# Kernel optimization log

Hardware: AMD Instinct MI355X
Metric: run time of the kernel (lower is better)

## Reference

```python
import jax, jax.numpy as jnp
import numpy as np

E = 1024  # embed_dim
H = 16    # heads
D = E // H            # head_dim = 64
M = 4 * D             # nb_features = 256
B, N = 4, 4096
KERNEL_EPS = 1e-4


def setup_inputs() -> dict:
    key = jax.random.key(0)
    ks = jax.random.split(key, 7)
    s = E ** -0.5
    return {
        "x": jax.random.normal(ks[0], (B, N, E), jnp.float32),
        "Wq": jax.random.normal(ks[1], (E, E), jnp.float32) * s,
        "bq": jnp.zeros((E,), jnp.float32),
        "Wk": jax.random.normal(ks[2], (E, E), jnp.float32) * s,
        "bk": jnp.zeros((E,), jnp.float32),
        "Wv": jax.random.normal(ks[3], (E, E), jnp.float32) * s,
        "bv": jnp.zeros((E,), jnp.float32),
        "Wo": jax.random.normal(ks[4], (E, E), jnp.float32) * s,
        "bo": jnp.zeros((E,), jnp.float32),
        "proj": jax.random.normal(ks[5], (M, D), jnp.float32),  # FAVOR+ random features
    }


def softmax_kernel(data, proj, is_query):
    # data: [B,H,N,D], proj: [M,D] -> features [B,H,N,M]
    d = data.shape[-1]
    data_n = data * (d ** -0.25)
    ratio = proj.shape[0] ** -0.5
    dd = jnp.einsum('bhnd,md->bhnm', data_n, proj)
    diag = 0.5 * jnp.sum(data_n * data_n, axis=-1, keepdims=True)
    if is_query:
        stab = jnp.max(dd, axis=-1, keepdims=True)
    else:
        stab = jnp.max(dd)
    return ratio * (jnp.exp(dd - diag - stab) + KERNEL_EPS)


def reference(x, Wq, bq, Wk, bk, Wv, bv, Wo, bo, proj):
    b, n, e = x.shape
    def split_heads(t):
        return t.reshape(b, n, H, D).transpose(0, 2, 1, 3)  # [B,H,N,D]
    q = split_heads(x @ Wq.T + bq)
    k = split_heads(x @ Wk.T + bk)
    v = split_heads(x @ Wv.T + bv)

    qf = softmax_kernel(q, proj, is_query=True)   # [B,H,N,M]
    kf = softmax_kernel(k, proj, is_query=False)  # [B,H,N,M]

    # non-causal linear attention: O(N*M*D)
    k_sum = jnp.sum(kf, axis=-2)                          # [B,H,M]
    d_inv = 1.0 / jnp.einsum('bhnm,bhm->bhn', qf, k_sum)  # [B,H,N]
    context = jnp.einsum('bhnm,bhnd->bhmd', kf, v)        # [B,H,M,D]
    out = jnp.einsum('bhnm,bhmd,bhn->bhnd', qf, context, d_inv)

    out = out.transpose(0, 2, 1, 3).reshape(b, n, e)
    return out @ Wo.T + bo
```

## Files before the change

kernel.cpp:

```cpp
#include <hip/hip_runtime.h>
#include <hip/hip_bf16.h>
#include <stdint.h>


#define TOKN  16384
#define SEQ   4096
#define EMB   1024
#define LDQ   3072
#define NHEAD 16
#define HD    64
#define NF    256
#define BHN   64

static __device__ __forceinline__ constexpr float c1f()  { return 0.35355339059327379f; }
static __device__ __forceinline__ constexpr float ratf() { return 0.0625f; }
static __device__ __forceinline__ constexpr float kepsf(){ return 1e-4f; }

typedef unsigned short u16;
typedef unsigned int   u32;
typedef __attribute__((ext_vector_type(8))) short bf16x8;
typedef __attribute__((ext_vector_type(4))) float f32x4;
typedef __attribute__((ext_vector_type(4))) u16   u16x4;

union U8 { bf16x8 v8; u16x4 q[2]; };

__device__ __forceinline__ float bf2f(u16 u) { return __uint_as_float(((u32)u) << 16); }
__device__ __forceinline__ u16 f2bf(float f) {
  u32 u = __float_as_uint(f);
  u += 0x7fffu + ((u >> 16) & 1u);
  return (u16)(u >> 16);
}
__device__ __forceinline__ u32 encf(float f) {
  u32 u = __float_as_uint(f);
  return (u & 0x80000000u) ? ~u : (u | 0x80000000u);
}
__device__ __forceinline__ float decf(u32 e) {
  u32 u = (e & 0x80000000u) ? (e & 0x7fffffffu) : ~e;
  return __uint_as_float(u);
}

__device__ __forceinline__ void gl2lds16(const u16* g, void* l) {
  __builtin_amdgcn_global_load_lds(
      (const __attribute__((address_space(1))) u32*)g,
      (__attribute__((address_space(3))) u32*)l, 16, 0, 0);
}

#define ZERO_ACC(acc)                         \
  _Pragma("unroll") for (int _i = 0; _i < 4; _i++) \
  _Pragma("unroll") for (int _j = 0; _j < 4; _j++) acc[_i][_j] = (f32x4)0.0f;

template <int BM, int BN>
__device__ __forceinline__ void gemm_core(const u16* __restrict__ Ag, long lda,
                                          const u16* __restrict__ Bg, long ldb,
                                          int K, u16* sA, u16* sB,
                                          f32x4 (&acc)[4][4]) {
  const int tid = threadIdx.x;
  const int w = tid >> 6, l = tid & 63;
  constexpr int WM = BM / 64;
  const int wm = w % WM, wn = w / WM;
  const int lrow = l & 15, g4 = l >> 4;
  constexpr int AI = (BM * 8) / 256;
  constexpr int BI = (BN * 8) / 256;
  static_assert(AI + BI == 8, "vmcnt(8) literal assumes 8 loads/thread/tile");
  constexpr int ABUF = BM * 64;
  constexpr int BBUF = BN * 64;

  auto stage = [&](int k0, int sel) {
#pragma unroll
    for (int i = 0; i < AI; i++) {
      int q = i * 256 + tid;
      int row = q >> 3, part = (q & 7) ^ (row & 7);
      gl2lds16(Ag + (long)row * lda + k0 + part * 8,
               (char*)(sA + sel * ABUF) + i * 4096 + w * 1024);
    }
#pragma unroll
    for (int i = 0; i < BI; i++) {
      int q = i * 256 + tid;
      int row = q >> 3, part = (q & 7) ^ (row & 7);
      gl2lds16(Bg + (long)row * ldb + k0 + part * 8,
               (char*)(sB + sel * BBUF) + i * 4096 + w * 1024);
    }
  };

  stage(0, 0);
  const int NT = K >> 6;
  for (int t = 0; t < NT; ++t) {
    const int sel = t & 1;
    if (t + 1 < NT) {
      stage((t + 1) * 64, sel ^ 1);
      asm volatile("s_waitcnt vmcnt(8)" ::: "memory");
    } else {
      asm volatile("s_waitcnt vmcnt(0)" ::: "memory");
    }
    __builtin_amdgcn_s_barrier();
    __builtin_amdgcn_sched_barrier(0);
    const u16* pA = sA + sel * ABUF;
    const u16* pB = sB + sel * BBUF;
#pragma unroll
    for (int kk = 0; kk < 2; kk++) {
      bf16x8 af[4], bfr[4];
#pragma unroll
      for (int mt = 0; mt < 4; mt++) {
        int row = wm * 64 + mt * 16 + lrow;
        af[mt] = *(const bf16x8*)(pA + row * 64 + (((kk * 4 + g4) ^ (row & 7)) * 8));
      }
#pragma unroll
      for (int nt = 0; nt < 4; nt++) {
        int row = wn * 64 + nt * 16 + lrow;
        bfr[nt] = *(const bf16x8*)(pB + row * 64 + (((kk * 4 + g4) ^ (row & 7)) * 8));
      }
#pragma unroll
      for (int mt = 0; mt < 4; mt++)
#pragma unroll
        for (int nt = 0; nt < 4; nt++)
          acc[mt][nt] = __builtin_amdgcn_mfma_f32_16x16x32_bf16(af[mt], bfr[nt], acc[mt][nt], 0, 0, 0);
    }
    __builtin_amdgcn_s_barrier();
  }
}

template <bool BF16OUT>
__global__ __launch_bounds__(256) void k_gemm(const u16* __restrict__ A, const u16* __restrict__ Bw,
                                              void* __restrict__ Cout, const float* __restrict__ bias,
                                              int K, int lda, int ldb, int ldc) {
  __shared__ __align__(16) u16 sA[2 * 128 * 64];
  __shared__ __align__(16) u16 sB[2 * 128 * 64];
  const int nbx = gridDim.x;
  const int nwg = nbx * gridDim.y;
  int lin = blockIdx.y * nbx + blockIdx.x;
  if ((nwg & 7) == 0) {
    int per = nwg >> 3;
    lin = (lin & 7) * per + (lin >> 3);
  }
  const int m0 = (lin / nbx) * 128, n0 = (lin % nbx) * 128;
  f32x4 acc[4][4]; ZERO_ACC(acc);
  gemm_core<128, 128>(A + (long)m0 * lda, lda, Bw + (long)n0 * ldb, ldb, K, sA, sB, acc);
  const int l = threadIdx.x & 63, w = threadIdx.x >> 6;
  const int wm = w & 1, wn = w >> 1, lr4 = (l >> 4) * 4, lc = l & 15;
#pragma unroll
  for (int nt = 0; nt < 4; nt++) {
    int gcol = n0 + wn * 64 + nt * 16 + lc;
    float bia = bias[gcol];
#pragma unroll
    for (int mt = 0; mt < 4; mt++)
#pragma unroll
      for (int r = 0; r < 4; r++) {
        int grow = m0 + wm * 64 + mt * 16 + lr4 + r;
        float v = acc[mt][nt][r] + bia;
        if (BF16OUT) ((u16*)Cout)[(long)grow * ldc + gcol] = f2bf(v);
        else         ((float*)Cout)[(long)grow * ldc + gcol] = v;
      }
  }
}

__global__ __launch_bounds__(256) void k_gemm3(const u16* __restrict__ A, const u16* __restrict__ Bw,
                                               u16* __restrict__ Cout,
                                               const float* __restrict__ b0, const float* __restrict__ b1,
                                               const float* __restrict__ b2,
                                               int K, int lda, int ldb, int ldc) {
  __shared__ __align__(16) u16 sA[2 * 128 * 64];
  __shared__ __align__(16) u16 sB[2 * 128 * 64];
  const int nbx = gridDim.x;
  const int nwg = nbx * gridDim.y;
  int lin = blockIdx.y * nbx + blockIdx.x;
  if ((nwg & 7) == 0) {
    int per = nwg >> 3;
    lin = (lin & 7) * per + (lin >> 3);
  }
  const int m0 = (lin / nbx) * 128, n0 = (lin % nbx) * 128;
  f32x4 acc[4][4]; ZERO_ACC(acc);
  gemm_core<128, 128>(A + (long)m0 * lda, lda, Bw + (long)n0 * ldb, ldb, K, sA, sB, acc);
  const int l = threadIdx.x & 63, w = threadIdx.x >> 6;
  const int wm = w & 1, wn = w >> 1, lr4 = (l >> 4) * 4, lc = l & 15;
  const int seg = n0 >> 10;
  const float* bias = seg == 0 ? b0 : (seg == 1 ? b1 : b2);
#pragma unroll
  for (int nt = 0; nt < 4; nt++) {
    int gcol = n0 + wn * 64 + nt * 16 + lc;
    float bia = bias[gcol & 1023];
#pragma unroll
    for (int mt = 0; mt < 4; mt++)
#pragma unroll
      for (int r = 0; r < 4; r++) {
        int grow = m0 + wm * 64 + mt * 16 + lr4 + r;
        Cout[(long)grow * ldc + gcol] = f2bf(acc[mt][nt][r] + bia);
      }
  }
}

__global__ __launch_bounds__(256) void k_vT(const u16* __restrict__ vb, u16* __restrict__ vT,
                                            float* __restrict__ vsum) {
  __shared__ u16 t[64][72];
  const int bh = blockIdx.y, n0 = blockIdx.x * 64, b = bh >> 4, h = bh & 15;
  const int tid = threadIdx.x;
#pragma unroll
  for (int i = 0; i < 2; i++) {
    int idx = i * 256 + tid, row = idx >> 3, c8 = idx & 7;
    U8 u;
    u.v8 = *(const bf16x8*)&vb[((long)(b * SEQ) + n0 + row) * LDQ + h * HD + c8 * 8];
    *(u16x4*)&t[row][c8 * 8]     = u.q[0];
    *(u16x4*)&t[row][c8 * 8 + 4] = u.q[1];
  }
  __syncthreads();
  const int nq = tid & 15, dh = tid >> 4;
#pragma unroll
  for (int i = 0; i < 4; i++) {
    int d = i * 16 + dh;
    u16x4 pk; float s = 0.f;
#pragma unroll
    for (int j = 0; j < 4; j++) { u16 v = t[nq * 4 + j][d]; pk[j] = v; s += bf2f(v); }
    *(u16x4*)&vT[((long)bh * HD + d) * SEQ + n0 + nq * 4] = pk;
    s += __shfl_xor(s, 1); s += __shfl_xor(s, 2);
    s += __shfl_xor(s, 4); s += __shfl_xor(s, 8);
    if (nq == 0) atomicAdd(&vsum[bh * HD + d], s);
  }
}

__global__ __launch_bounds__(256, 2) void k_fk_ctx(const u16* __restrict__ kb, const u16* __restrict__ vT,
                                                   const u16* __restrict__ projb, u16* __restrict__ part,
                                                   float* __restrict__ su, u32* __restrict__ stabEnc) {
  __shared__ __align__(16) u16 sU[4][64 * 64];
  const int ck = blockIdx.x, bh = blockIdx.y, b = bh >> 4, h = bh & 15;
  const int tid = threadIdx.x, w = tid >> 6, l = tid & 63;
  const int c = l & 15, g = l >> 4;
  u16* sUw = &sU[w][0];
  const int sw = c & 7;

  bf16x8 pf[4][2];
#pragma unroll
  for (int nt = 0; nt < 4; nt++)
#pragma unroll
    for (int k0 = 0; k0 < 2; k0++)
      pf[nt][k0] = *(const bf16x8*)&projb[(w * 64 + nt * 16 + c) * 64 + k0 * 32 + g * 8];

  f32x4 acc2[4][4]; ZERO_ACC(acc2);
  float suv[4] = {0.f, 0.f, 0.f, 0.f};
  float amax = -1e30f;
  const long tok0 = (long)b * SEQ + ck * 256;

  for (int s = 0; s < 4; s++) {
    const long t0 = tok0 + s * 64;
    bf16x8 af[4][2];
#pragma unroll
    for (int mt = 0; mt < 4; mt++)
#pragma unroll
      for (int k0 = 0; k0 < 2; k0++)
        af[mt][k0] = *(const bf16x8*)&kb[(t0 + mt * 16 + c) * LDQ + h * HD + k0 * 32 + g * 8];
    bf16x8 vf[2][4];
#pragma unroll
    for (int k0 = 0; k0 < 2; k0++)
#pragma unroll
      for (int nt = 0; nt < 4; nt++)
        vf[k0][nt] = *(const bf16x8*)&vT[((long)bh * HD + nt * 16 + c) * SEQ +
                                         ck * 256 + s * 64 + k0 * 32 + g * 8];

#pragma unroll
    for (int mt = 0; mt < 4; mt++) {
      float ss = 0.f;
#pragma unroll
      for (int k0 = 0; k0 < 2; k0++)
#pragma unroll
        for (int j = 0; j < 8; j++) {
          float v = bf2f((u16)af[mt][k0][j]);
          ss += v * v;
        }
      ss += __shfl_xor(ss, 16);
      ss += __shfl_xor(ss, 32);
      const float dgrow = ss * 0.0625f;
      f32x4 accR[4];
#pragma unroll
      for (int nt = 0; nt < 4; nt++) accR[nt] = (f32x4)0.0f;
#pragma unroll
      for (int k0 = 0; k0 < 2; k0++)
#pragma unroll
        for (int nt = 0; nt < 4; nt++)
          accR[nt] = __builtin_amdgcn_mfma_f32_16x16x32_bf16(af[mt][k0], pf[nt][k0], accR[nt], 0, 0, 0);
      float dg[4];
#pragma unroll
      for (int r = 0; r < 4; r++) dg[r] = __shfl(dgrow, g * 4 + r);
#pragma unroll
      for (int nt = 0; nt < 4; nt++) {
        u16x4 pk;
#pragma unroll
        for (int r = 0; r < 4; r++) {
          float a = accR[nt][r];
          amax = fmaxf(amax, a);
          float U = __expf(fmaf(a, c1f(), -dg[r]));
          pk[r] = f2bf(U);
          suv[nt] += U;
        }
        *(u16x4*)&sUw[(nt * 16 + c) * 64 + (((mt * 2 + (g >> 1)) ^ sw) * 2 + (g & 1)) * 4] = pk;
      }
    }
#pragma unroll
    for (int k0 = 0; k0 < 2; k0++) {
      bf16x8 uf[4];
#pragma unroll
      for (int mt = 0; mt < 4; mt++)
        uf[mt] = *(const bf16x8*)&sUw[(mt * 16 + c) * 64 + ((k0 * 4 + g) ^ sw) * 8];
#pragma unroll
      for (int mt = 0; mt < 4; mt++)
#pragma unroll
        for (int nt = 0; nt < 4; nt++)
          acc2[mt][nt] = __builtin_amdgcn_mfma_f32_16x16x32_bf16(uf[mt], vf[k0][nt], acc2[mt][nt], 0, 0, 0);
    }
  }
  const long zp = (long)(bh * 16 + ck);
#pragma unroll
  for (int mt = 0; mt < 4; mt++)
#pragma unroll
    for (int nt = 0; nt < 4; nt++)
#pragma unroll
      for (int r = 0; r < 4; r++) {
        int m = w * 64 + mt * 16 + g * 4 + r;
        int d = nt * 16 + c;
        part[(zp * NF + m) * HD + d] = f2bf(acc2[mt][nt][r]);
      }
#pragma unroll
  for (int nt = 0; nt < 4; nt++) {
    float v = suv[nt];
    v += __shfl_xor(v, 16);
    v += __shfl_xor(v, 32);
    if (l < 16) atomicAdd(&su[bh * NF + w * 64 + nt * 16 + l], v);
  }
  for (int o = 32; o; o >>= 1) amax = fmaxf(amax, __shfl_xor(amax, o));
  if (l == 0) atomicMax(stabEnc, encf(c1f() * amax));
}

__global__ __launch_bounds__(256, 4) void k_fq_attn(const u16* __restrict__ qb, const u16* __restrict__ projb,
                                                    const float* __restrict__ k_sum, const float* __restrict__ ksum_tot,
                                                    const u16* __restrict__ ct_bf, const float* __restrict__ ctsum,
                                                    u16* __restrict__ attn_bf) {
  __shared__ __align__(16) u16 sUq[64 * 256];
  __shared__ float redmax[4][64];
  __shared__ float redsum[4][64];
  const int bh = blockIdx.y, b = bh >> 4, h = bh & 15;
  const long t0 = (long)b * SEQ + blockIdx.x * 64;
  const int tid = threadIdx.x, w = tid >> 6, l = tid & 63;
  const int lrow = l & 15, lk = (l >> 4) * 8, lr4 = (l >> 4) * 4, lc = l & 15;

  bf16x8 pf[4][2];
#pragma unroll
  for (int mt = 0; mt < 4; mt++)
#pragma unroll
    for (int k0 = 0; k0 < 2; k0++)
      pf[mt][k0] = *(const bf16x8*)&projb[(w * 64 + mt * 16 + lrow) * 64 + k0 * 32 + lk];
  bf16x8 af[4][2];
#pragma unroll
  for (int nt = 0; nt < 4; nt++)
#pragma unroll
    for (int k0 = 0; k0 < 2; k0++)
      af[nt][k0] = *(const bf16x8*)&qb[(t0 + nt * 16 + lrow) * LDQ + h * HD + k0 * 32 + lk];

  float dgq[4];
#pragma unroll
  for (int nt = 0; nt < 4; nt++) {
    float ss = 0.f;
#pragma unroll
    for (int k0 = 0; k0 < 2; k0++)
#pragma unroll
      for (int j = 0; j < 8; j++) {
        float v = bf2f((u16)af[nt][k0][j]);
        ss += v * v;
      }
    ss += __shfl_xor(ss, 16);
    ss += __shfl_xor(ss, 32);
    dgq[nt] = ss * 0.0625f;
  }

  f32x4 ksr[4];
#pragma unroll
  for (int mt = 0; mt < 4; mt++)
    ksr[mt] = *(const f32x4*)&k_sum[(long)bh * NF + w * 64 + mt * 16 + lr4];

#pragma unroll
  for (int nt = 0; nt < 4; nt++) {
    f32x4 accC[4];
#pragma unroll
    for (int mt = 0; mt < 4; mt++) accC[mt] = (f32x4)0.0f;
#pragma unroll
    for (int k0 = 0; k0 < 2; k0++)
#pragma unroll
      for (int mt = 0; mt < 4; mt++)
        accC[mt] = __builtin_amdgcn_mfma_f32_16x16x32_bf16(pf[mt][k0], af[nt][k0], accC[mt], 0, 0, 0);

    const int tok = nt * 16 + lc;
    const int trow = tok * NF, tsw = tok & 7;
    float vmax = -1e30f, s = 0.f;
#pragma unroll
    for (int mt = 0; mt < 4; mt++) {
      const int fb = w * 64 + mt * 16 + lr4;
      u16x4 pk;
#pragma unroll
      for (int r = 0; r < 4; r++) {
        float dd = c1f() * accC[mt][r];
        vmax = fmaxf(vmax, dd);
        float U = __expf(dd - dgq[nt]);
        pk[r] = f2bf(U);
        s += U * ksr[mt][r];
      }
      *(u16x4*)&sUq[trow + (((fb >> 3) ^ tsw) << 3) + (fb & 7)] = pk;
    }
    vmax = fmaxf(vmax, __shfl_xor(vmax, 16));
    vmax = fmaxf(vmax, __shfl_xor(vmax, 32));
    s += __shfl_xor(s, 16);
    s += __shfl_xor(s, 32);
    if (l < 16) { redmax[w][nt * 16 + l] = vmax; redsum[w][nt * 16 + l] = s; }
  }
  __syncthreads();
  f32x4 acc2[4];
#pragma unroll
  for (int mt = 0; mt < 4; mt++) acc2[mt] = (f32x4)0.0f;
#pragma unroll
  for (int kk = 0; kk < 8; kk++) {
    bf16x8 bfr = *(const bf16x8*)&ct_bf[((long)bh * HD + w * 16 + lrow) * NF + kk * 32 + lk];
#pragma unroll
    for (int mt = 0; mt < 4; mt++) {
      int row = mt * 16 + lrow;
      bf16x8 a2 = *(const bf16x8*)&sUq[row * NF + (((kk * 4 + (l >> 4)) ^ (row & 7)) * 8)];
      acc2[mt] = __builtin_amdgcn_mfma_f32_16x16x32_bf16(a2, bfr, acc2[mt], 0, 0, 0);
    }
  }
  const float kst = ksum_tot[bh];
  const float cts = ctsum[(long)bh * HD + w * 16 + lc];
#pragma unroll
  for (int mt = 0; mt < 4; mt++)
#pragma unroll
    for (int r = 0; r < 4; r++) {
      int row = mt * 16 + lr4 + r;
      float rs = fmaxf(fmaxf(redmax[0][row], redmax[1][row]),
                       fmaxf(redmax[2][row], redmax[3][row]));
      float S1 = redsum[0][row] + redsum[1][row] + redsum[2][row] + redsum[3][row];
      float ers = __expf(-rs);
      float di = 1.0f / (ratf() * (ers * S1 + kepsf() * kst));
      float a_ = di * ratf() * ers;
      float b_ = di * ratf() * kepsf();
      float ov = a_ * acc2[mt][r] + b_ * cts;
      attn_bf[(t0 + row) * EMB + h * HD + w * 16 + lc] = f2bf(ov);
    }
}

__global__ void k_cvt(const float* __restrict__ s, u16* __restrict__ d, long n4) {
  long i = (long)blockIdx.x * blockDim.x + threadIdx.x;
  if (i >= n4) return;
  float4 v = ((const float4*)s)[i];
  u16x4 o = { f2bf(v.x), f2bf(v.y), f2bf(v.z), f2bf(v.w) };
  ((u16x4*)d)[i] = o;
}

__global__ void k_init(float* su, float* vsum, u32* stabEnc) {
  int i = blockIdx.x * 256 + threadIdx.x;
  if (i < BHN * NF) su[i] = 0.f;
  if (i < BHN * HD) vsum[i] = 0.f;
  if (i == 0) *stabEnc = 0u;
}

__global__ __launch_bounds__(256) void k_asm_ksum(const float* __restrict__ su, const u32* __restrict__ stabEnc,
                                                  float* __restrict__ k_sum, float* __restrict__ ksum_tot) {
  __shared__ float red[256];
  int z = blockIdx.x, m = threadIdx.x;
  float es = __expf(-decf(*stabEnc));
  float v = ratf() * (es * su[(long)z * NF + m] + kepsf() * (float)SEQ);
  k_sum[(long)z * NF + m] = v;
  red[m] = v;
  __syncthreads();
  for (int s = 128; s > 0; s >>= 1) {
    if (m < s) red[m] += red[m + s];
    __syncthreads();
  }
  if (m == 0) ksum_tot[z] = red[0];
}

__global__ __launch_bounds__(256) void k_asm_ct(const u16* __restrict__ part, const float* __restrict__ vsum,
                                                const u32* __restrict__ stabEnc, u16* __restrict__ ct_bf,
                                                float* __restrict__ ctsum) {
  __shared__ float red[4][64];
  const int z = blockIdx.x, tid = threadIdx.x;
  const int w = tid >> 6, l = tid & 63;
  float es = __expf(-decf(*stabEnc));
  float vs = vsum[(long)z * HD + l];
  float csum = 0.f;
  for (int m = w; m < NF; m += 4) {
    float a = 0.f;
#pragma unroll
    for (int ck = 0; ck < 16; ck++)
      a += bf2f(part[((long)(z * 16 + ck) * NF + m) * HD + l]);
    float cv = ratf() * (es * a + kepsf() * vs);
    ct_bf[((long)z * HD + l) * NF + m] = f2bf(cv);
    csum += cv;
  }
  red[w][l] = csum;
  __syncthreads();
  if (tid < 64)
    ctsum[(long)z * HD + tid] = red[0][tid] + red[1][tid] + red[2][tid] + red[3][tid];
}

extern "C" void kernel_launch(void* const* d_in, const int* in_sizes, int n_in,
                              void* d_out, int out_size, void* d_ws, size_t ws_size,
                              hipStream_t stream) {
  const float* x    = (const float*)d_in[0];
  const float* Wq   = (const float*)d_in[1];
  const float* bq   = (const float*)d_in[2];
  const float* Wk   = (const float*)d_in[3];
  const float* bk   = (const float*)d_in[4];
  const float* Wv   = (const float*)d_in[5];
  const float* bv   = (const float*)d_in[6];
  const float* Wo   = (const float*)d_in[7];
  const float* bo   = (const float*)d_in[8];
  const float* proj = (const float*)d_in[9];

  char* base = (char*)d_ws;
  size_t off = 0;
  auto alloc = [&](size_t bytes) {
    off = (off + 255) & ~(size_t)255;
    char* r = base + off;
    off += bytes;
    return r;
  };
  u16*  xb     = (u16*)alloc((size_t)TOKN * EMB * 2);
  u16*  wqkv   = (u16*)alloc((size_t)3 * EMB * EMB * 2);
  u16*  wob    = (u16*)alloc((size_t)EMB * EMB * 2);
  u16*  projb  = (u16*)alloc((size_t)NF * HD * 2);
  u16*  qkv    = (u16*)alloc((size_t)TOKN * LDQ * 2);
  float* su    = (float*)alloc((size_t)BHN * NF * 4);
  float* k_sum = (float*)alloc((size_t)BHN * NF * 4);
  float* ksum_t= (float*)alloc((size_t)BHN * 4);
  float* vsum  = (float*)alloc((size_t)BHN * HD * 4);
  float* ctsum = (float*)alloc((size_t)BHN * HD * 4);
  u32*  stabE  = (u32*)alloc(256);
  u16*  ct_bf  = (u16*)alloc((size_t)BHN * HD * NF * 2);
  u16*  qb     = qkv;
  u16*  kb     = qkv + EMB;
  u16*  vb     = qkv + 2 * EMB;
  u16*  part   = xb;
  u16*  attn_bf= xb;
  u16*  vT     = (u16*)d_out;

  k_init<<<64, 256, 0, stream>>>(su, vsum, stabE);
  k_cvt<<<(TOKN * EMB / 4 + 255) / 256, 256, 0, stream>>>(x, xb, (long)TOKN * EMB / 4);
  k_cvt<<<(EMB * EMB / 4 + 255) / 256, 256, 0, stream>>>(Wq, wqkv, (long)EMB * EMB / 4);
  k_cvt<<<(EMB * EMB / 4 + 255) / 256, 256, 0, stream>>>(Wk, wqkv + (size_t)EMB * EMB, (long)EMB * EMB / 4);
  k_cvt<<<(EMB * EMB / 4 + 255) / 256, 256, 0, stream>>>(Wv, wqkv + (size_t)2 * EMB * EMB, (long)EMB * EMB / 4);
  k_cvt<<<(EMB * EMB / 4 + 255) / 256, 256, 0, stream>>>(Wo, wob, (long)EMB * EMB / 4);
  k_cvt<<<(NF * HD / 4 + 255) / 256, 256, 0, stream>>>(proj, projb, (long)NF * HD / 4);
  k_gemm3<<<dim3(LDQ / 128, TOKN / 128), 256, 0, stream>>>(xb, wqkv, qkv, bq, bk, bv,
                                                           EMB, EMB, EMB, LDQ);
  k_vT<<<dim3(SEQ / 64, BHN), 256, 0, stream>>>(vb, vT, vsum);
  k_fk_ctx<<<dim3(16, BHN), 256, 0, stream>>>(kb, vT, projb, part, su, stabE);
  k_asm_ksum<<<BHN, 256, 0, stream>>>(su, stabE, k_sum, ksum_t);
  k_asm_ct<<<BHN, 256, 0, stream>>>(part, vsum, stabE, ct_bf, ctsum);
  k_fq_attn<<<dim3(SEQ / 64, BHN), 256, 0, stream>>>(qb, projb, k_sum, ksum_t, ct_bf, ctsum, attn_bf);
  k_gemm<false><<<dim3(EMB / 128, TOKN / 128), 256, 0, stream>>>(attn_bf, wob, d_out, bo, EMB, EMB, EMB, EMB);
}
```

Before: 501.9 us.

## Fuse V transpose and sum into QKV GEMM epilogue, merge conversion kernels

The QKV GEMM epilogue now writes the V segment directly in transposed [B,H,D,N] layout and accumulates the per-head V sums with shuffles and atomics. This removes the separate k_vT pass and the V columns of the qkv buffer, which shrinks its leading dimension to 2048. All fp32-to-bf16 conversions and the buffer zeroing are merged into one launch to cut launch overhead. The transposed stores are 8-byte chunks strided by SEQ, so they may coalesce poorly, and the atomics add contention.

```diff
diff --git a/kernel.cpp b/kernel.cpp
--- a/kernel.cpp
+++ b/kernel.cpp
@@ -6,7 +6,7 @@
 #define TOKN  16384
 #define SEQ   4096
 #define EMB   1024
-#define LDQ   3072
+#define LDQ   2048
 #define NHEAD 16
 #define HD    64
 #define NF    256
@@ -157,6 +157,7 @@
                                                u16* __restrict__ Cout,
                                                const float* __restrict__ b0, const float* __restrict__ b1,
                                                const float* __restrict__ b2,
+                                               u16* __restrict__ vTout, float* __restrict__ vsum,
                                                int K, int lda, int ldb, int ldc) {
   __shared__ __align__(16) u16 sA[2 * 128 * 64];
   __shared__ __align__(16) u16 sB[2 * 128 * 64];
@@ -173,46 +174,45 @@
   const int l = threadIdx.x & 63, w = threadIdx.x >> 6;
   const int wm = w & 1, wn = w >> 1, lr4 = (l >> 4) * 4, lc = l & 15;
   const int seg = n0 >> 10;
-  const float* bias = seg == 0 ? b0 : (seg == 1 ? b1 : b2);
-#pragma unroll
-  for (int nt = 0; nt < 4; nt++) {
-    int gcol = n0 + wn * 64 + nt * 16 + lc;
-    float bia = bias[gcol & 1023];
-#pragma unroll
-    for (int mt = 0; mt < 4; mt++)
-#pragma unroll
-      for (int r = 0; r < 4; r++) {
-        int grow = m0 + wm * 64 + mt * 16 + lr4 + r;
-        Cout[(long)grow * ldc + gcol] = f2bf(acc[mt][nt][r] + bia);
-      }
-  }
-}
-
-__global__ __launch_bounds__(256) void k_vT(const u16* __restrict__ vb, u16* __restrict__ vT,
-                                            float* __restrict__ vsum) {
-  __shared__ u16 t[64][72];
-  const int bh = blockIdx.y, n0 = blockIdx.x * 64, b = bh >> 4, h = bh & 15;
-  const int tid = threadIdx.x;
-#pragma unroll
-  for (int i = 0; i < 2; i++) {
-    int idx = i * 256 + tid, row = idx >> 3, c8 = idx & 7;
-    U8 u;
-    u.v8 = *(const bf16x8*)&vb[((long)(b * SEQ) + n0 + row) * LDQ + h * HD + c8 * 8];
-    *(u16x4*)&t[row][c8 * 8]     = u.q[0];
-    *(u16x4*)&t[row][c8 * 8 + 4] = u.q[1];
-  }
-  __syncthreads();
-  const int nq = tid & 15, dh = tid >> 4;
-#pragma unroll
-  for (int i = 0; i < 4; i++) {
-    int d = i * 16 + dh;
-    u16x4 pk; float s = 0.f;
-#pragma unroll
-    for (int j = 0; j < 4; j++) { u16 v = t[nq * 4 + j][d]; pk[j] = v; s += bf2f(v); }
-    *(u16x4*)&vT[((long)bh * HD + d) * SEQ + n0 + nq * 4] = pk;
-    s += __shfl_xor(s, 1); s += __shfl_xor(s, 2);
-    s += __shfl_xor(s, 4); s += __shfl_xor(s, 8);
-    if (nq == 0) atomicAdd(&vsum[bh * HD + d], s);
+  if (seg < 2) {
+    const float* bias = seg == 0 ? b0 : b1;
+#pragma unroll
+    for (int nt = 0; nt < 4; nt++) {
+      int gcol = n0 + wn * 64 + nt * 16 + lc;
+      float bia = bias[gcol & 1023];
+#pragma unroll
+      for (int mt = 0; mt < 4; mt++)
+#pragma unroll
+        for (int r = 0; r < 4; r++) {
+          int grow = m0 + wm * 64 + mt * 16 + lr4 + r;
+          Cout[(long)grow * ldc + gcol] = f2bf(acc[mt][nt][r] + bia);
+        }
+    }
+  } else {
+    const int b = m0 >> 12;
+#pragma unroll
+    for (int nt = 0; nt < 4; nt++) {
+      int e = (n0 & 1023) + wn * 64 + nt * 16 + lc;
+      int hh = e >> 6, d = e & 63;
+      float bia = b2[e];
+      long vbase = ((long)((b * 16 + hh) * 64 + d)) * SEQ;
+      float s = 0.f;
+#pragma unroll
+      for (int mt = 0; mt < 4; mt++) {
+        int grow0 = m0 + wm * 64 + mt * 16 + lr4;
+        u16x4 pk;
+#pragma unroll
+        for (int r = 0; r < 4; r++) {
+          float v = acc[mt][nt][r] + bia;
+          pk[r] = f2bf(v);
+          s += v;
+        }
+        *(u16x4*)&vTout[vbase + (grow0 & 4095)] = pk;
+      }
+      s += __shfl_xor(s, 16);
+      s += __shfl_xor(s, 32);
+      if (l < 16) atomicAdd(&vsum[(b * 16 + hh) * 64 + d], s);
+    }
   }
 }
 
@@ -440,19 +440,38 @@
     }
 }
 
-__global__ void k_cvt(const float* __restrict__ s, u16* __restrict__ d, long n4) {
-  long i = (long)blockIdx.x * blockDim.x + threadIdx.x;
-  if (i >= n4) return;
-  float4 v = ((const float4*)s)[i];
+#define NF4_X (TOKN * EMB / 4)
+#define NF4_W (EMB * EMB / 4)
+#define NF4_P (NF * HD / 4)
+__global__ void k_cvt_all(const float* __restrict__ x,
+                          const float* __restrict__ Wq, const float* __restrict__ Wk,
+                          const float* __restrict__ Wv, const float* __restrict__ Wo,
+                          const float* __restrict__ proj,
+                          u16* __restrict__ xb, u16* __restrict__ wqkv,
+                          u16* __restrict__ wob, u16* __restrict__ projb,
+                          float* __restrict__ su, float* __restrict__ vsum,
+                          u32* __restrict__ stabEnc) {
+  const long b0 = NF4_X;
+  const long b1 = b0 + NF4_W, b2 = b1 + NF4_W, b3 = b2 + NF4_W, b4 = b3 + NF4_W;
+  const long b5 = b4 + NF4_P;
+  long i = (long)blockIdx.x * 256 + threadIdx.x;
+  const float* s; u16* d; long off;
+  if      (i < b0) { s = x;    d = xb;                          off = i; }
+  else if (i < b1) { s = Wq;   d = wqkv;                        off = i - b0; }
+  else if (i < b2) { s = Wk;   d = wqkv + (size_t)EMB * EMB;    off = i - b1; }
+  else if (i < b3) { s = Wv;   d = wqkv + (size_t)2 * EMB * EMB; off = i - b2; }
+  else if (i < b4) { s = Wo;   d = wob;                         off = i - b3; }
+  else if (i < b5) { s = proj; d = projb;                       off = i - b4; }
+  else {
+    long j = i - b5;
+    if (j < BHN * NF) su[j] = 0.f;
+    else if (j < BHN * NF + BHN * HD) vsum[j - BHN * NF] = 0.f;
+    else if (j == BHN * NF + BHN * HD) *stabEnc = 0u;
+    return;
+  }
+  float4 v = ((const float4*)s)[off];
   u16x4 o = { f2bf(v.x), f2bf(v.y), f2bf(v.z), f2bf(v.w) };
-  ((u16x4*)d)[i] = o;
-}
-
-__global__ void k_init(float* su, float* vsum, u32* stabEnc) {
-  int i = blockIdx.x * 256 + threadIdx.x;
-  if (i < BHN * NF) su[i] = 0.f;
-  if (i < BHN * HD) vsum[i] = 0.f;
-  if (i == 0) *stabEnc = 0u;
+  ((u16x4*)d)[off] = o;
 }
 
 __global__ __launch_bounds__(256) void k_asm_ksum(const float* __restrict__ su, const u32* __restrict__ stabEnc,
@@ -530,22 +549,18 @@
   u32*  stabE  = (u32*)alloc(256);
   u16*  ct_bf  = (u16*)alloc((size_t)BHN * HD * NF * 2);
   u16*  qb     = qkv;
-  u16*  kb     = qkv + EMB;
-  u16*  vb     = qkv + 2 * EMB;
+  u16*  kb     = qkv + 1024;
   u16*  part   = xb;
   u16*  attn_bf= xb;
   u16*  vT     = (u16*)d_out;
 
-  k_init<<<64, 256, 0, stream>>>(su, vsum, stabE);
-  k_cvt<<<(TOKN * EMB / 4 + 255) / 256, 256, 0, stream>>>(x, xb, (long)TOKN * EMB / 4);
-  k_cvt<<<(EMB * EMB / 4 + 255) / 256, 256, 0, stream>>>(Wq, wqkv, (long)EMB * EMB / 4);
-  k_cvt<<<(EMB * EMB / 4 + 255) / 256, 256, 0, stream>>>(Wk, wqkv + (size_t)EMB * EMB, (long)EMB * EMB / 4);
-  k_cvt<<<(EMB * EMB / 4 + 255) / 256, 256, 0, stream>>>(Wv, wqkv + (size_t)2 * EMB * EMB, (long)EMB * EMB / 4);
-  k_cvt<<<(EMB * EMB / 4 + 255) / 256, 256, 0, stream>>>(Wo, wob, (long)EMB * EMB / 4);
-  k_cvt<<<(NF * HD / 4 + 255) / 256, 256, 0, stream>>>(proj, projb, (long)NF * HD / 4);
-  k_gemm3<<<dim3(LDQ / 128, TOKN / 128), 256, 0, stream>>>(xb, wqkv, qkv, bq, bk, bv,
-                                                           EMB, EMB, EMB, LDQ);
-  k_vT<<<dim3(SEQ / 64, BHN), 256, 0, stream>>>(vb, vT, vsum);
+  {
+    const long total = (long)NF4_X + 4 * NF4_W + NF4_P + BHN * NF + BHN * HD + 1;
+    k_cvt_all<<<(unsigned)((total + 255) / 256), 256, 0, stream>>>(
+        x, Wq, Wk, Wv, Wo, proj, xb, wqkv, wob, projb, su, vsum, stabE);
+  }
+  k_gemm3<<<dim3(3072 / 128, TOKN / 128), 256, 0, stream>>>(xb, wqkv, qkv, bq, bk, bv,
+                                                            vT, vsum, EMB, EMB, EMB, LDQ);
   k_fk_ctx<<<dim3(16, BHN), 256, 0, stream>>>(kb, vT, projb, part, su, stabE);
   k_asm_ksum<<<BHN, 256, 0, stream>>>(su, stabE, k_sum, ksum_t);
   k_asm_ct<<<BHN, 256, 0, stream>>>(part, vsum, stabE, ct_bf, ctsum);
```

Measured after the change: 472.6 us. -5.8%, faster.
